# Optimization experiments

Measured on AMD Instinct MI355X. Metric: run time of the kernel, lower is better.

## Reference

```python
import jax, jax.numpy as jnp
import numpy as np

HEADS = 24
HEAD_DIM = 128
DIM = HEADS * HEAD_DIM  # 3072
EPS = 1e-5


def _rms_norm(x, w):
    # x: [B,S,H,D], w: [D]
    var = jnp.mean(jnp.square(x), axis=-1, keepdims=True)
    return x * jax.lax.rsqrt(var + EPS) * w


def _apply_rope(x, cos, sin):
    # non-neox (interleaved pairs): x: [B,S,H,D], cos/sin: [S,D]
    B, S, H, D = x.shape
    xr = x.reshape(B, S, H, D // 2, 2)
    x_real, x_imag = xr[..., 0], xr[..., 1]
    rotated = jnp.stack([-x_imag, x_real], axis=-1).reshape(B, S, H, D)
    c = cos[None, :, None, :]
    s = sin[None, :, None, :]
    return x * c + rotated * s


def setup_inputs() -> dict:
    key = jax.random.key(0)
    ks = jax.random.split(key, 20)
    B, S_img, S_txt = 1, 2048, 512
    S = S_img + S_txt
    sc = 1.0 / np.sqrt(DIM)
    inp = {
        "x": jax.random.normal(ks[0], (B, S_img, DIM), jnp.float32),
        "encoder_hidden_states": jax.random.normal(ks[1], (B, S_txt, DIM), jnp.float32),
        "rope_cos": jax.random.uniform(ks[2], (S, HEAD_DIM), jnp.float32),
        "rope_sin": jax.random.uniform(ks[3], (S, HEAD_DIM), jnp.float32),
        # image-stream projections (bias=False)
        "wq": jax.random.normal(ks[4], (DIM, DIM), jnp.float32) * sc,
        "wk": jax.random.normal(ks[5], (DIM, DIM), jnp.float32) * sc,
        "wv": jax.random.normal(ks[6], (DIM, DIM), jnp.float32) * sc,
        # text-stream projections (added_proj_bias=True)
        "w_add_q": jax.random.normal(ks[7], (DIM, DIM), jnp.float32) * sc,
        "w_add_k": jax.random.normal(ks[8], (DIM, DIM), jnp.float32) * sc,
        "w_add_v": jax.random.normal(ks[9], (DIM, DIM), jnp.float32) * sc,
        "b_add_q": jax.random.normal(ks[10], (DIM,), jnp.float32) * 0.01,
        "b_add_k": jax.random.normal(ks[11], (DIM,), jnp.float32) * 0.01,
        "b_add_v": jax.random.normal(ks[12], (DIM,), jnp.float32) * 0.01,
        # per-head RMSNorm weights
        "norm_q_w": jnp.ones((HEAD_DIM,), jnp.float32),
        "norm_k_w": jnp.ones((HEAD_DIM,), jnp.float32),
        "norm_aq_w": jnp.ones((HEAD_DIM,), jnp.float32),
        "norm_ak_w": jnp.ones((HEAD_DIM,), jnp.float32),
        # output projections (out_bias=True)
        "w_out": jax.random.normal(ks[13], (DIM, DIM), jnp.float32) * sc,
        "b_out": jax.random.normal(ks[14], (DIM,), jnp.float32) * 0.01,
        "w_add_out": jax.random.normal(ks[15], (DIM, DIM), jnp.float32) * sc,
        "b_add_out": jax.random.normal(ks[16], (DIM,), jnp.float32) * 0.01,
    }
    return inp


def reference(x, encoder_hidden_states, rope_cos, rope_sin,
              wq, wk, wv, w_add_q, w_add_k, w_add_v,
              b_add_q, b_add_k, b_add_v,
              norm_q_w, norm_k_w, norm_aq_w, norm_ak_w,
              w_out, b_out, w_add_out, b_add_out):
    B, S_img, _ = x.shape
    S_txt = encoder_hidden_states.shape[1]

    def proj(h, w, b=None):
        y = jnp.einsum('bsd,ed->bse', h, w)
        return y if b is None else y + b

    def heads(t):
        return t.reshape(B, t.shape[1], HEADS, HEAD_DIM)

    q = _rms_norm(heads(proj(x, wq)), norm_q_w)
    k = _rms_norm(heads(proj(x, wk)), norm_k_w)
    v = heads(proj(x, wv))

    eq = _rms_norm(heads(proj(encoder_hidden_states, w_add_q, b_add_q)), norm_aq_w)
    ek = _rms_norm(heads(proj(encoder_hidden_states, w_add_k, b_add_k)), norm_ak_w)
    ev = heads(proj(encoder_hidden_states, w_add_v, b_add_v))

    # encoder tokens first, then image tokens
    q = jnp.concatenate([eq, q], axis=1)
    k = jnp.concatenate([ek, k], axis=1)
    v = jnp.concatenate([ev, v], axis=1)

    q = _apply_rope(q, rope_cos, rope_sin)
    k = _apply_rope(k, rope_cos, rope_sin)

    scale = 1.0 / np.sqrt(HEAD_DIM)
    scores = jnp.einsum('bqhd,bkhd->bhqk', q, k) * scale
    attn = jax.nn.softmax(scores, axis=-1)
    o = jnp.einsum('bhqk,bkhd->bqhd', attn, v)
    o = o.reshape(B, S_txt + S_img, DIM)

    enc_o, img_o = o[:, :S_txt], o[:, S_txt:]
    img_out = jnp.einsum('bsd,ed->bse', img_o, w_out) + b_out
    enc_out = jnp.einsum('bsd,ed->bse', enc_o, w_add_out) + b_add_out
    return img_out, enc_out
```

## Files before the change

### kernel.cpp

```cpp
#include <hip/hip_runtime.h>
#include <hip/hip_bf16.h>


typedef __hip_bfloat16 bf16;
typedef __attribute__((ext_vector_type(8))) short short8;
typedef __attribute__((ext_vector_type(4))) short s16x4;
typedef __attribute__((ext_vector_type(4))) float f32x4;

#define KDIM 3072
#define S_TXT 512
#define S_IMG 2048
#define S_ALL 2560
#define NHEADS 24
#define HDIM 128
#define WELEM (KDIM * KDIM)
#define AELEM (S_ALL * KDIM)
#define NSPLIT 3

__device__ __forceinline__ void async_ld16(const void* g, void* l) {
  __builtin_amdgcn_global_load_lds((__attribute__((address_space(1))) void*)g,
                                   (__attribute__((address_space(3))) void*)l,
                                   16, 0, 0);
}

__device__ __forceinline__ short bf16_bits(float x) {
  bf16 h = (bf16)x;
  return __builtin_bit_cast(short, h);
}
__device__ __forceinline__ float bits_f32(short s) {
  return (float)__builtin_bit_cast(bf16, s);
}

__global__ __launch_bounds__(256) void cast_weights_kernel(
    const float* __restrict__ w0, const float* __restrict__ w1,
    const float* __restrict__ w2, const float* __restrict__ w3,
    const float* __restrict__ w4, const float* __restrict__ w5,
    const float* __restrict__ w6, const float* __restrict__ w7,
    bf16* __restrict__ dst) {
  const float* srcs[8] = {w0, w1, w2, w3, w4, w5, w6, w7};
  const float* __restrict__ src = srcs[blockIdx.y];
  bf16* __restrict__ out = dst + (size_t)blockIdx.y * WELEM;
  const size_t i0 = ((size_t)blockIdx.x * 256 + threadIdx.x) * 8;
  const float4 f0 = *(const float4*)(src + i0);
  const float4 f1 = *(const float4*)(src + i0 + 4);
  short8 o;
  o[0] = bf16_bits(f0.x); o[1] = bf16_bits(f0.y);
  o[2] = bf16_bits(f0.z); o[3] = bf16_bits(f0.w);
  o[4] = bf16_bits(f1.x); o[5] = bf16_bits(f1.y);
  o[6] = bf16_bits(f1.z); o[7] = bf16_bits(f1.w);
  *(short8*)(out + i0) = o;
}

__global__ __launch_bounds__(256) void cast_acts_kernel(
    const float* __restrict__ x, const float* __restrict__ enc,
    bf16* __restrict__ xe) {
  const size_t i0 = ((size_t)blockIdx.x * 256 + threadIdx.x) * 8;
  const size_t TXT = (size_t)S_TXT * KDIM;
  const float* __restrict__ src = (i0 < TXT) ? (enc + i0) : (x + (i0 - TXT));
  const float4 f0 = *(const float4*)(src);
  const float4 f1 = *(const float4*)(src + 4);
  short8 o;
  o[0] = bf16_bits(f0.x); o[1] = bf16_bits(f0.y);
  o[2] = bf16_bits(f0.z); o[3] = bf16_bits(f0.w);
  o[4] = bf16_bits(f1.x); o[5] = bf16_bits(f1.y);
  o[6] = bf16_bits(f1.z); o[7] = bf16_bits(f1.w);
  *(short8*)(xe + i0) = o;
}

template <typename OutT, bool TRANS>
__device__ __forceinline__ void gemm_tile(const bf16* __restrict__ A,
                                          const bf16* __restrict__ B,
                                          OutT* __restrict__ C,
                                          const float* __restrict__ bias) {
  __shared__ alignas(16) short sA[128 * 32];
  __shared__ alignas(16) short sB[128 * 32];
  const int tid = threadIdx.x;
  const int lane = tid & 63;
  const int w = tid >> 6;
  const int a = lane & 15;
  const int g = lane >> 4;
  const int wm = (w >> 1) * 64;
  const int wn = (w & 1) * 64;

  f32x4 acc[4][4] = {};

  const int s0 = tid, s1 = tid + 256;
  const bf16* gA0 = A + (s0 >> 2) * KDIM + (s0 & 3) * 8;
  const bf16* gA1 = A + (s1 >> 2) * KDIM + (s1 & 3) * 8;
  const bf16* gB0 = B + (s0 >> 2) * KDIM + (s0 & 3) * 8;
  const bf16* gB1 = B + (s1 >> 2) * KDIM + (s1 & 3) * 8;
  short* lA0 = sA + (w * 64) * 8;
  short* lA1 = sA + (256 + w * 64) * 8;
  short* lB0 = sB + (w * 64) * 8;
  short* lB1 = sB + (256 + w * 64) * 8;

  for (int k0 = 0; k0 < KDIM; k0 += 32) {
    __syncthreads();
    async_ld16(gA0 + k0, lA0);
    async_ld16(gA1 + k0, lA1);
    async_ld16(gB0 + k0, lB0);
    async_ld16(gB1 + k0, lB1);
    __syncthreads();
    short8 af[4], bfg[4];
#pragma unroll
    for (int i = 0; i < 4; i++)
      af[i] = *(const short8*)(sA + (wm + i * 16 + a) * 32 + g * 8);
#pragma unroll
    for (int j = 0; j < 4; j++)
      bfg[j] = *(const short8*)(sB + (wn + j * 16 + a) * 32 + g * 8);
#pragma unroll
    for (int i = 0; i < 4; i++)
#pragma unroll
      for (int j = 0; j < 4; j++)
        acc[i][j] = __builtin_amdgcn_mfma_f32_16x16x32_bf16(af[i], bfg[j], acc[i][j], 0, 0, 0);
  }

  if constexpr (TRANS) {
#pragma unroll
    for (int i = 0; i < 4; i++)
#pragma unroll
      for (int j = 0; j < 4; j++) {
        const int col = wn + j * 16 + a;
        const float bv = bias ? bias[col] : 0.0f;
        s16x4 pk;
#pragma unroll
        for (int r = 0; r < 4; r++) pk[r] = bf16_bits(acc[i][j][r] + bv);
        *(s16x4*)((short*)C + (size_t)col * S_ALL + wm + i * 16 + g * 4) = pk;
      }
  } else {
#pragma unroll
    for (int i = 0; i < 4; i++)
#pragma unroll
      for (int j = 0; j < 4; j++) {
        const int col = wn + j * 16 + a;
        const float bv = bias ? bias[col] : 0.0f;
#pragma unroll
        for (int r = 0; r < 4; r++) {
          const int row = wm + i * 16 + g * 4 + r;
          C[(size_t)row * KDIM + col] = (OutT)(acc[i][j][r] + bv);
        }
      }
  }
}

__global__ __launch_bounds__(256) void qkv_kernel(
    const bf16* __restrict__ XE, const bf16* __restrict__ Wc,
    const float* __restrict__ bq, const float* __restrict__ bk, const float* __restrict__ bv,
    bf16* __restrict__ Q, bf16* __restrict__ K, bf16* __restrict__ VT) {
  const int bm = blockIdx.x;
  const int bn = blockIdx.y;
  const int which = bn / 24;
  const int nc = (bn % 24) * 128;
  const bool txt = bm < 4;
  const bf16* W = Wc + (size_t)(txt ? (3 + which) : which) * WELEM + (size_t)nc * KDIM;
  const float* bias = nullptr;
  if (txt) bias = ((which == 0) ? bq : (which == 1) ? bk : bv) + nc;
  const int crow = bm * 128;
  const bf16* A = XE + (size_t)crow * KDIM;
  if (which == 2) {
    gemm_tile<bf16, true>(A, W, VT + (size_t)nc * S_ALL + crow, bias);
  } else {
    bf16* Out = (which == 0) ? Q : K;
    gemm_tile<bf16, false>(A, W, Out + (size_t)crow * KDIM + nc, bias);
  }
}

__global__ __launch_bounds__(256) void outproj_kernel(
    const bf16* __restrict__ Obuf, const bf16* __restrict__ Wc,
    const float* __restrict__ b_out, const float* __restrict__ b_add,
    float* __restrict__ out) {
  const int bm = blockIdx.x;
  const int bn = blockIdx.y;
  const bool txt = bm < 4;
  const bf16* A = Obuf + (size_t)bm * 128 * KDIM;
  const bf16* W = Wc + (size_t)(txt ? 7 : 6) * WELEM;
  const float* bias = txt ? b_add : b_out;
  float* C = txt ? (out + (size_t)S_IMG * KDIM + (size_t)bm * 128 * KDIM)
                 : (out + (size_t)(bm - 4) * 128 * KDIM);
  gemm_tile<float, false>(A, W + (size_t)bn * 128 * KDIM, C + bn * 128, bias + bn * 128);
}

__global__ __launch_bounds__(256) void norm_rope_kernel(
    bf16* __restrict__ Q, bf16* __restrict__ K,
    const float* __restrict__ rc, const float* __restrict__ rs,
    const float* __restrict__ nqw, const float* __restrict__ nkw,
    const float* __restrict__ naqw, const float* __restrict__ nakw) {
  const int row = blockIdx.x;
  const int h = blockIdx.y * 4 + (threadIdx.x >> 6);
  const int t = threadIdx.x & 63;
  const long base = (long)row * KDIM + h * HDIM;
  const int d0 = 2 * t, d1 = d0 + 1;
  const bool txt = row < S_TXT;
  const float QSCL = 0.08838834764831845f * 1.4426950408889634f;
  float qa = (float)Q[base + d0], qb = (float)Q[base + d1];
  float ka = (float)K[base + d0], kb = (float)K[base + d1];
  float sq = qa * qa + qb * qb;
  float sk = ka * ka + kb * kb;
#pragma unroll
  for (int m = 1; m < 64; m <<= 1) {
    sq += __shfl_xor(sq, m);
    sk += __shfl_xor(sk, m);
  }
  const float rq = rsqrtf(sq * (1.0f / 128.0f) + 1e-5f) * QSCL;
  const float rk = rsqrtf(sk * (1.0f / 128.0f) + 1e-5f);
  const float* qw = txt ? naqw : nqw;
  const float* kw = txt ? nakw : nkw;
  const float c0 = rc[row * HDIM + d0], c1 = rc[row * HDIM + d1];
  const float s0 = rs[row * HDIM + d0], s1 = rs[row * HDIM + d1];
  const float qn0 = qa * rq * qw[d0], qn1 = qb * rq * qw[d1];
  const float kn0 = ka * rk * kw[d0], kn1 = kb * rk * kw[d1];
  Q[base + d0] = (bf16)(qn0 * c0 - qn1 * s0);
  Q[base + d1] = (bf16)(qn1 * c1 + qn0 * s1);
  K[base + d0] = (bf16)(kn0 * c0 - kn1 * s0);
  K[base + d1] = (bf16)(kn1 * c1 + kn0 * s1);
}

__global__ __launch_bounds__(256) void flash_kernel(
    const bf16* __restrict__ Q, const bf16* __restrict__ Kb,
    const bf16* __restrict__ VT,
    bf16* __restrict__ Op0, bf16* __restrict__ Op1, bf16* __restrict__ Op2,
    float* __restrict__ L) {
  __shared__ alignas(16) short sK[64 * 128];
  __shared__ alignas(16) short sVT[128 * 64];
  __shared__ alignas(16) short sP[4][32 * 72];
  const int tid = threadIdx.x;
  const int lane = tid & 63;
  const int w = tid >> 6;
  const int a = lane & 15;
  const int g = lane >> 4;
  const int qt = blockIdx.x;
  const int h = blockIdx.y;
  const int split = blockIdx.z;
  const int it0 = split * 13;
  const int it1 = (split == 2) ? 40 : (it0 + 13);
  const int qrow0 = qt * 128 + w * 32;
  short* const sPw = sP[w];

  short8 qf[2][4];
#pragma unroll
  for (int mi = 0; mi < 2; mi++)
#pragma unroll
    for (int kk = 0; kk < 4; kk++)
      qf[mi][kk] = *(const short8*)(Q + (size_t)(qrow0 + mi * 16 + a) * KDIM + h * HDIM + kk * 32 + g * 8);

  f32x4 oacc[2][8] = {};
  float lsum[2] = {0.0f, 0.0f};

  for (int it = it0; it < it1; ++it) {
    const int kv0 = it * 64;
    __syncthreads();
#pragma unroll
    for (int is = 0; is < 4; is++) {
      const int s = is * 256 + w * 64 + lane;
      const int kr = s >> 4, p = s & 15;
      const int lb = (p - (kr & 7)) & 15;
      async_ld16(Kb + (size_t)(kv0 + kr) * KDIM + h * HDIM + lb * 8,
                 sK + (is * 256 + w * 64) * 8);
    }
#pragma unroll
    for (int is = 0; is < 4; is++) {
      const int s = is * 256 + w * 64 + lane;
      const int dr = s >> 3, p = s & 7;
      const int lb = (p - (dr & 7)) & 7;
      async_ld16(VT + (size_t)(h * HDIM + dr) * S_ALL + kv0 + lb * 8,
                 sVT + (is * 256 + w * 64) * 8);
    }
    __syncthreads();

    f32x4 st[4][2] = {};
#pragma unroll
    for (int kk = 0; kk < 4; kk++) {
      short8 kf[4];
#pragma unroll
      for (int ni = 0; ni < 4; ni++) {
        const int kr = ni * 16 + a;
        const int p = ((kk * 4 + g) + (kr & 7)) & 15;
        kf[ni] = *(const short8*)(sK + kr * 128 + p * 8);
      }
#pragma unroll
      for (int ni = 0; ni < 4; ni++)
#pragma unroll
        for (int mi = 0; mi < 2; mi++)
          st[ni][mi] = __builtin_amdgcn_mfma_f32_16x16x32_bf16(kf[ni], qf[mi][kk], st[ni][mi], 0, 0, 0);
    }

#pragma unroll
    for (int mi = 0; mi < 2; mi++)
#pragma unroll
      for (int ni = 0; ni < 4; ni++) {
        s16x4 pk;
#pragma unroll
        for (int r = 0; r < 4; r++) {
          const float p = exp2f(st[ni][mi][r]);
          lsum[mi] += p;
          pk[r] = bf16_bits(p);
        }
        *(s16x4*)(sPw + (mi * 16 + a) * 72 + ni * 16 + g * 4) = pk;
      }

#pragma unroll
    for (int ks = 0; ks < 2; ks++) {
      short8 pf[2];
#pragma unroll
      for (int mi = 0; mi < 2; mi++)
        pf[mi] = *(const short8*)(sPw + (mi * 16 + a) * 72 + ks * 32 + g * 8);
#pragma unroll
      for (int nd = 0; nd < 8; nd++) {
        const int dr = nd * 16 + a;
        const int p = ((ks * 4 + g) + (dr & 7)) & 7;
        const short8 vf = *(const short8*)(sVT + dr * 64 + p * 8);
#pragma unroll
        for (int mi = 0; mi < 2; mi++)
          oacc[mi][nd] = __builtin_amdgcn_mfma_f32_16x16x32_bf16(pf[mi], vf, oacc[mi][nd], 0, 0, 0);
      }
    }
  }

#pragma unroll
  for (int mi = 0; mi < 2; mi++) {
    lsum[mi] += __shfl_xor(lsum[mi], 16);
    lsum[mi] += __shfl_xor(lsum[mi], 32);
  }
  bf16* __restrict__ Op = (split == 0) ? Op0 : (split == 1) ? Op1 : Op2;
#pragma unroll
  for (int mi = 0; mi < 2; mi++) {
#pragma unroll
    for (int r = 0; r < 4; r++) {
      const float inv = 1.0f / __shfl(lsum[mi], g * 4 + r);
      const size_t row = qrow0 + mi * 16 + g * 4 + r;
#pragma unroll
      for (int nd = 0; nd < 8; nd++)
        Op[row * KDIM + h * HDIM + nd * 16 + a] = (bf16)(oacc[mi][nd][r] * inv);
    }
    if (g == 0)
      L[((size_t)split * NHEADS + h) * S_ALL + qrow0 + mi * 16 + a] = lsum[mi];
  }
}

__global__ __launch_bounds__(256) void merge_kernel(
    bf16* __restrict__ O0, const bf16* __restrict__ O1, const bf16* __restrict__ O2,
    const float* __restrict__ L) {
  const size_t i0 = ((size_t)blockIdx.x * 256 + threadIdx.x) * 8;
  const int row = (int)(i0 / KDIM);
  const int h = (int)((i0 % KDIM) >> 7);
  const float l0 = L[((size_t)0 * NHEADS + h) * S_ALL + row];
  const float l1 = L[((size_t)1 * NHEADS + h) * S_ALL + row];
  const float l2 = L[((size_t)2 * NHEADS + h) * S_ALL + row];
  const float inv = 1.0f / (l0 + l1 + l2);
  const float w0 = l0 * inv, w1 = l1 * inv, w2 = l2 * inv;
  const short8 v0 = *(const short8*)(O0 + i0);
  const short8 v1 = *(const short8*)(O1 + i0);
  const short8 v2 = *(const short8*)(O2 + i0);
  short8 o;
#pragma unroll
  for (int u = 0; u < 8; u++)
    o[u] = bf16_bits(w0 * bits_f32(v0[u]) + w1 * bits_f32(v1[u]) + w2 * bits_f32(v2[u]));
  *(short8*)(O0 + i0) = o;
}

extern "C" void kernel_launch(void* const* d_in, const int* in_sizes, int n_in,
                              void* d_out, int out_size, void* d_ws, size_t ws_size,
                              hipStream_t stream) {
  const float* x    = (const float*)d_in[0];
  const float* enc  = (const float*)d_in[1];
  const float* rc   = (const float*)d_in[2];
  const float* rs   = (const float*)d_in[3];
  const float* wq   = (const float*)d_in[4];
  const float* wk   = (const float*)d_in[5];
  const float* wv   = (const float*)d_in[6];
  const float* waq  = (const float*)d_in[7];
  const float* wak  = (const float*)d_in[8];
  const float* wav  = (const float*)d_in[9];
  const float* bq   = (const float*)d_in[10];
  const float* bk   = (const float*)d_in[11];
  const float* bv   = (const float*)d_in[12];
  const float* nqw  = (const float*)d_in[13];
  const float* nkw  = (const float*)d_in[14];
  const float* naqw = (const float*)d_in[15];
  const float* nakw = (const float*)d_in[16];
  const float* w_out     = (const float*)d_in[17];
  const float* b_out     = (const float*)d_in[18];
  const float* w_add_out = (const float*)d_in[19];
  const float* b_add_out = (const float*)d_in[20];

  bf16* Wc   = (bf16*)d_ws;
  bf16* XE   = Wc + (size_t)8 * WELEM;
  bf16* Q    = XE + AELEM;
  bf16* K    = Q + AELEM;
  bf16* VT   = K + AELEM;
  bf16* Obuf = VT + AELEM;
  bf16* Op1  = Obuf + AELEM;
  bf16* Op2  = XE;
  float* L   = (float*)(Op1 + AELEM);

  cast_weights_kernel<<<dim3(WELEM / 2048, 8), 256, 0, stream>>>(
      wq, wk, wv, waq, wak, wav, w_out, w_add_out, Wc);
  cast_acts_kernel<<<dim3(AELEM / 2048), 256, 0, stream>>>(x, enc, XE);

  qkv_kernel<<<dim3(20, 72), 256, 0, stream>>>(XE, Wc, bq, bk, bv, Q, K, VT);
  norm_rope_kernel<<<dim3(S_ALL, 6), 256, 0, stream>>>(Q, K, rc, rs, nqw, nkw, naqw, nakw);
  flash_kernel<<<dim3(20, NHEADS, NSPLIT), 256, 0, stream>>>(Q, K, VT, Obuf, Op1, Op2, L);
  merge_kernel<<<dim3(AELEM / 2048), 256, 0, stream>>>(Obuf, Op1, Op2, L);
  outproj_kernel<<<dim3(20, NHEADS), 256, 0, stream>>>(Obuf, Wc, b_out, b_add_out,
                                                       (float*)d_out);
}
```

Baseline: 759.3 us.

## Fuse weight fp32-to-bf16 cast into GEMM tile loads with swizzled LDS

Removes the separate weight cast kernel. The GEMMs now read fp32 weights directly, convert them to bf16 in registers and store them to LDS. An XOR swizzle is added to the LDS layout of both A and B tiles to reduce bank conflicts. This saves writing and rereading eight bf16 weight matrices. In exchange each weight tile is converted repeatedly across the row blocks (20 for the QKV kernel), fp32 global reads double the B-side bytes, and the B loads become synchronous register loads instead of async LDS loads.

Result: slower. 872.8 us (+14.9%).

```diff
diff --git a/kernel.cpp b/kernel.cpp
--- a/kernel.cpp
+++ b/kernel.cpp
@@ -13,7 +13,6 @@
 #define S_ALL 2560
 #define NHEADS 24
 #define HDIM 128
-#define WELEM (KDIM * KDIM)
 #define AELEM (S_ALL * KDIM)
 #define NSPLIT 3
 
@@ -29,26 +28,6 @@
 }
 __device__ __forceinline__ float bits_f32(short s) {
   return (float)__builtin_bit_cast(bf16, s);
-}
-
-__global__ __launch_bounds__(256) void cast_weights_kernel(
-    const float* __restrict__ w0, const float* __restrict__ w1,
-    const float* __restrict__ w2, const float* __restrict__ w3,
-    const float* __restrict__ w4, const float* __restrict__ w5,
-    const float* __restrict__ w6, const float* __restrict__ w7,
-    bf16* __restrict__ dst) {
-  const float* srcs[8] = {w0, w1, w2, w3, w4, w5, w6, w7};
-  const float* __restrict__ src = srcs[blockIdx.y];
-  bf16* __restrict__ out = dst + (size_t)blockIdx.y * WELEM;
-  const size_t i0 = ((size_t)blockIdx.x * 256 + threadIdx.x) * 8;
-  const float4 f0 = *(const float4*)(src + i0);
-  const float4 f1 = *(const float4*)(src + i0 + 4);
-  short8 o;
-  o[0] = bf16_bits(f0.x); o[1] = bf16_bits(f0.y);
-  o[2] = bf16_bits(f0.z); o[3] = bf16_bits(f0.w);
-  o[4] = bf16_bits(f1.x); o[5] = bf16_bits(f1.y);
-  o[6] = bf16_bits(f1.z); o[7] = bf16_bits(f1.w);
-  *(short8*)(out + i0) = o;
 }
 
 __global__ __launch_bounds__(256) void cast_acts_kernel(
@@ -69,7 +48,7 @@
 
 template <typename OutT, bool TRANS>
 __device__ __forceinline__ void gemm_tile(const bf16* __restrict__ A,
-                                          const bf16* __restrict__ B,
+                                          const float* __restrict__ B,
                                           OutT* __restrict__ C,
                                           const float* __restrict__ bias) {
   __shared__ alignas(16) short sA[128 * 32];
@@ -85,29 +64,50 @@
   f32x4 acc[4][4] = {};
 
   const int s0 = tid, s1 = tid + 256;
-  const bf16* gA0 = A + (s0 >> 2) * KDIM + (s0 & 3) * 8;
-  const bf16* gA1 = A + (s1 >> 2) * KDIM + (s1 & 3) * 8;
-  const bf16* gB0 = B + (s0 >> 2) * KDIM + (s0 & 3) * 8;
-  const bf16* gB1 = B + (s1 >> 2) * KDIM + (s1 & 3) * 8;
+  const int r0 = s0 >> 2, b0 = (s0 & 3) ^ ((r0 >> 1) & 3);
+  const int r1 = s1 >> 2, b1 = (s1 & 3) ^ ((r1 >> 1) & 3);
+  const bf16* gA0 = A + (size_t)r0 * KDIM + b0 * 8;
+  const bf16* gA1 = A + (size_t)r1 * KDIM + b1 * 8;
   short* lA0 = sA + (w * 64) * 8;
   short* lA1 = sA + (256 + w * 64) * 8;
-  short* lB0 = sB + (w * 64) * 8;
-  short* lB1 = sB + (256 + w * 64) * 8;
+
+  const int brow = tid >> 1, bh = tid & 1;
+  const float* gB = B + (size_t)brow * KDIM + bh * 16;
+  const int bsw = (brow >> 1) & 3;
+  short* lB0 = sB + brow * 32 + (((bh * 2 + 0) ^ bsw) * 8);
+  short* lB1 = sB + brow * 32 + (((bh * 2 + 1) ^ bsw) * 8);
 
   for (int k0 = 0; k0 < KDIM; k0 += 32) {
     __syncthreads();
     async_ld16(gA0 + k0, lA0);
     async_ld16(gA1 + k0, lA1);
-    async_ld16(gB0 + k0, lB0);
-    async_ld16(gB1 + k0, lB1);
+    const float4 f0 = *(const float4*)(gB + k0);
+    const float4 f1 = *(const float4*)(gB + k0 + 4);
+    const float4 f2 = *(const float4*)(gB + k0 + 8);
+    const float4 f3 = *(const float4*)(gB + k0 + 12);
+    short8 p0, p1;
+    p0[0] = bf16_bits(f0.x); p0[1] = bf16_bits(f0.y);
+    p0[2] = bf16_bits(f0.z); p0[3] = bf16_bits(f0.w);
+    p0[4] = bf16_bits(f1.x); p0[5] = bf16_bits(f1.y);
+    p0[6] = bf16_bits(f1.z); p0[7] = bf16_bits(f1.w);
+    p1[0] = bf16_bits(f2.x); p1[1] = bf16_bits(f2.y);
+    p1[2] = bf16_bits(f2.z); p1[3] = bf16_bits(f2.w);
+    p1[4] = bf16_bits(f3.x); p1[5] = bf16_bits(f3.y);
+    p1[6] = bf16_bits(f3.z); p1[7] = bf16_bits(f3.w);
+    *(short8*)lB0 = p0;
+    *(short8*)lB1 = p1;
     __syncthreads();
     short8 af[4], bfg[4];
 #pragma unroll
-    for (int i = 0; i < 4; i++)
-      af[i] = *(const short8*)(sA + (wm + i * 16 + a) * 32 + g * 8);
-#pragma unroll
-    for (int j = 0; j < 4; j++)
-      bfg[j] = *(const short8*)(sB + (wn + j * 16 + a) * 32 + g * 8);
+    for (int i = 0; i < 4; i++) {
+      const int R = wm + i * 16 + a;
+      af[i] = *(const short8*)(sA + R * 32 + ((g ^ ((R >> 1) & 3)) * 8));
+    }
+#pragma unroll
+    for (int j = 0; j < 4; j++) {
+      const int R = wn + j * 16 + a;
+      bfg[j] = *(const short8*)(sB + R * 32 + ((g ^ ((R >> 1) & 3)) * 8));
+    }
 #pragma unroll
     for (int i = 0; i < 4; i++)
 #pragma unroll
@@ -144,7 +144,9 @@
 }
 
 __global__ __launch_bounds__(256) void qkv_kernel(
-    const bf16* __restrict__ XE, const bf16* __restrict__ Wc,
+    const bf16* __restrict__ XE,
+    const float* __restrict__ wq, const float* __restrict__ wk, const float* __restrict__ wv,
+    const float* __restrict__ waq, const float* __restrict__ wak, const float* __restrict__ wav,
     const float* __restrict__ bq, const float* __restrict__ bk, const float* __restrict__ bv,
     bf16* __restrict__ Q, bf16* __restrict__ K, bf16* __restrict__ VT) {
   const int bm = blockIdx.x;
@@ -152,7 +154,11 @@
   const int which = bn / 24;
   const int nc = (bn % 24) * 128;
   const bool txt = bm < 4;
-  const bf16* W = Wc + (size_t)(txt ? (3 + which) : which) * WELEM + (size_t)nc * KDIM;
+  const float* W;
+  if (which == 0)      W = txt ? waq : wq;
+  else if (which == 1) W = txt ? wak : wk;
+  else                 W = txt ? wav : wv;
+  W += (size_t)nc * KDIM;
   const float* bias = nullptr;
   if (txt) bias = ((which == 0) ? bq : (which == 1) ? bk : bv) + nc;
   const int crow = bm * 128;
@@ -166,14 +172,15 @@
 }
 
 __global__ __launch_bounds__(256) void outproj_kernel(
-    const bf16* __restrict__ Obuf, const bf16* __restrict__ Wc,
-    const float* __restrict__ b_out, const float* __restrict__ b_add,
+    const bf16* __restrict__ Obuf,
+    const float* __restrict__ w_out, const float* __restrict__ b_out,
+    const float* __restrict__ w_add, const float* __restrict__ b_add,
     float* __restrict__ out) {
   const int bm = blockIdx.x;
   const int bn = blockIdx.y;
   const bool txt = bm < 4;
   const bf16* A = Obuf + (size_t)bm * 128 * KDIM;
-  const bf16* W = Wc + (size_t)(txt ? 7 : 6) * WELEM;
+  const float* W = txt ? w_add : w_out;
   const float* bias = txt ? b_add : b_out;
   float* C = txt ? (out + (size_t)S_IMG * KDIM + (size_t)bm * 128 * KDIM)
                  : (out + (size_t)(bm - 4) * 128 * KDIM);
@@ -383,8 +390,7 @@
   const float* w_add_out = (const float*)d_in[19];
   const float* b_add_out = (const float*)d_in[20];
 
-  bf16* Wc   = (bf16*)d_ws;
-  bf16* XE   = Wc + (size_t)8 * WELEM;
+  bf16* XE   = (bf16*)d_ws;
   bf16* Q    = XE + AELEM;
   bf16* K    = Q + AELEM;
   bf16* VT   = K + AELEM;
@@ -393,14 +399,12 @@
   bf16* Op2  = XE;
   float* L   = (float*)(Op1 + AELEM);
 
-  cast_weights_kernel<<<dim3(WELEM / 2048, 8), 256, 0, stream>>>(
-      wq, wk, wv, waq, wak, wav, w_out, w_add_out, Wc);
   cast_acts_kernel<<<dim3(AELEM / 2048), 256, 0, stream>>>(x, enc, XE);
-
-  qkv_kernel<<<dim3(20, 72), 256, 0, stream>>>(XE, Wc, bq, bk, bv, Q, K, VT);
+  qkv_kernel<<<dim3(20, 72), 256, 0, stream>>>(XE, wq, wk, wv, waq, wak, wav,
+                                               bq, bk, bv, Q, K, VT);
   norm_rope_kernel<<<dim3(S_ALL, 6), 256, 0, stream>>>(Q, K, rc, rs, nqw, nkw, naqw, nakw);
   flash_kernel<<<dim3(20, NHEADS, NSPLIT), 256, 0, stream>>>(Q, K, VT, Obuf, Op1, Op2, L);
   merge_kernel<<<dim3(AELEM / 2048), 256, 0, stream>>>(Obuf, Op1, Op2, L);
-  outproj_kernel<<<dim3(20, NHEADS), 256, 0, stream>>>(Obuf, Wc, b_out, b_add_out,
-                                                       (float*)d_out);
-}
+  outproj_kernel<<<dim3(20, NHEADS), 256, 0, stream>>>(Obuf, w_out, b_out,
+                                                       w_add_out, b_add_out, (float*)d_out);
+}
```
